# Performance work log

Hardware: AMD Instinct MI355X
Metric: run time of the kernel (lower is better)

## Reference

```python
import jax, jax.numpy as jnp
import numpy as np

D_MODEL = 768
N_HEADS = 12
D_HEAD = D_MODEL // N_HEADS
D_FF = 3072
EPS = 1e-5


def setup_inputs() -> dict:
    key = jax.random.key(0)
    ks = jax.random.split(key, 12)
    s = 0.02
    return {
        "x": jax.random.normal(ks[0], (2, 2048, D_MODEL), dtype=jnp.float32),
        "ln1_g": jnp.ones((D_MODEL,), jnp.float32),
        "ln1_b": jnp.zeros((D_MODEL,), jnp.float32),
        "ln2_g": jnp.ones((D_MODEL,), jnp.float32),
        "ln2_b": jnp.zeros((D_MODEL,), jnp.float32),
        "w_qkv": jax.random.normal(ks[1], (D_MODEL, 3 * D_MODEL), jnp.float32) * s,
        "b_qkv": jnp.zeros((3 * D_MODEL,), jnp.float32),
        "w_out": jax.random.normal(ks[2], (D_MODEL, D_MODEL), jnp.float32) * s,
        "b_out": jnp.zeros((D_MODEL,), jnp.float32),
        "w_fc1": jax.random.normal(ks[3], (D_MODEL, D_FF), jnp.float32) * s,
        "b_fc1": jnp.zeros((D_FF,), jnp.float32),
        "w_fc2": jax.random.normal(ks[4], (D_FF, D_MODEL), jnp.float32) * s,
        "b_fc2": jnp.zeros((D_MODEL,), jnp.float32),
    }


def _layernorm(x, g, b):
    mu = jnp.mean(x, axis=-1, keepdims=True)
    var = jnp.var(x, axis=-1, keepdims=True)
    return (x - mu) * jax.lax.rsqrt(var + EPS) * g + b


def _attention(h, w_qkv, b_qkv, w_out, b_out):
    B, S, _ = h.shape
    qkv = h @ w_qkv + b_qkv  # [B,S,3D]
    qkv = qkv.reshape(B, S, 3, N_HEADS, D_HEAD)
    q, k, v = qkv[:, :, 0], qkv[:, :, 1], qkv[:, :, 2]  # [B,S,H,Dh]
    scale = 1.0 / np.sqrt(D_HEAD).astype(np.float32)
    scores = jnp.einsum("bqhd,bkhd->bhqk", q, k) * scale
    causal = jnp.tril(jnp.ones((S, S), bool))
    scores = jnp.where(causal[None, None], scores, -jnp.inf)
    attn = jax.nn.softmax(scores, axis=-1)
    out = jnp.einsum("bhqk,bkhd->bqhd", attn, v).reshape(B, S, D_MODEL)
    return out @ w_out + b_out


def reference(x, ln1_g, ln1_b, ln2_g, ln2_b, w_qkv, b_qkv, w_out, b_out,
              w_fc1, b_fc1, w_fc2, b_fc2):
    # x = x + Attention(LN1(x))
    x = x + _attention(_layernorm(x, ln1_g, ln1_b), w_qkv, b_qkv, w_out, b_out)
    # x = x + FFN(LN2(x)); GELU is exact (erf) to match torch nn.GELU default
    h = _layernorm(x, ln2_g, ln2_b)
    h = jax.nn.gelu(h @ w_fc1 + b_fc1, approximate=False) @ w_fc2 + b_fc2
    return x + h
```

## Files before the change

### kernel.cpp

```cpp
#include <hip/hip_runtime.h>
#include <hip/hip_bf16.h>

typedef unsigned short u16;
typedef unsigned int u32;
typedef unsigned char u8;
using short8 = __attribute__((ext_vector_type(8))) short;
using f32x4  = __attribute__((ext_vector_type(4))) float;
using float4v = __attribute__((ext_vector_type(4))) float;

__device__ __forceinline__ u16 f2bf(float f) {
    __hip_bfloat16 h = __float2bfloat16(f);
    union { __hip_bfloat16 h; u16 u; } cv; cv.h = h; return cv.u;
}
__device__ __forceinline__ float bf2f(u16 u) {
    union { u32 u; float f; } cv; cv.u = ((u32)u) << 16; return cv.f;
}
__device__ __forceinline__ u16 f2bf_trunc(float f) {
    union { float f; u32 u; } cv; cv.f = f; return (u16)(cv.u >> 16);
}

__device__ __forceinline__ void gload_lds16(const void* g, void* l) {
    __builtin_amdgcn_global_load_lds(
        (const __attribute__((address_space(1))) u32*)g,
        (__attribute__((address_space(3))) u32*)l, 16, 0, 0);
}

__global__ __launch_bounds__(256) void transpose_w(const float* __restrict__ W,
                                                   u16* __restrict__ Wt, int K, int N) {
    __shared__ float tile[32][33];
    int n0 = blockIdx.x * 32, k0 = blockIdx.y * 32;
    int tx = threadIdx.x & 31, ty = threadIdx.x >> 5;
    for (int i = 0; i < 4; i++) {
        int k = ty + i * 8;
        tile[k][tx] = W[(long)(k0 + k) * N + n0 + tx];
    }
    __syncthreads();
    for (int i = 0; i < 4; i++) {
        int n = ty + i * 8;
        Wt[(long)(n0 + n) * K + k0 + tx] = f2bf(tile[tx][n]);
    }
}

__global__ __launch_bounds__(256) void transpose_v(const u16* __restrict__ qkv,
                                                   u16* __restrict__ Vt) {
    __shared__ u16 tile[64][72];
    int s0 = blockIdx.x * 64;
    int bh = blockIdx.y;
    int b = bh / 12, h = bh % 12;
    int tid = threadIdx.x;
    const u16* src = qkv + (long)b * 2048 * 2304 + 1536 + h * 64;
    #pragma unroll
    for (int j = 0; j < 2; ++j) {
        int c = tid + j * 256;
        int srow = c >> 3, ch = c & 7;
        *(short8*)&tile[srow][ch * 8] = *(const short8*)(src + (long)(s0 + srow) * 2304 + ch * 8);
    }
    __syncthreads();
    u16* dst = Vt + (long)bh * 64 * 2048 + s0;
    #pragma unroll
    for (int j = 0; j < 2; ++j) {
        int c = tid + j * 256;
        int d = c >> 3, ch = c & 7;
        short8 v;
        #pragma unroll
        for (int e = 0; e < 8; ++e) v[e] = (short)tile[ch * 8 + e][d];
        *(short8*)(dst + (long)d * 2048 + ch * 8) = v;
    }
}

__global__ __launch_bounds__(256) void ln_kernel(const float* __restrict__ x,
                                                 const float* __restrict__ gain,
                                                 const float* __restrict__ beta,
                                                 u16* __restrict__ out) {
    int row = blockIdx.x;
    const float* xr = x + (long)row * 768;
    int tid = threadIdx.x;
    float v[3];
    float s = 0.f, s2 = 0.f;
    for (int j = 0; j < 3; j++) {
        v[j] = xr[tid + 256 * j];
        s += v[j]; s2 += v[j] * v[j];
    }
    for (int off = 32; off; off >>= 1) {
        s  += __shfl_down(s, off);
        s2 += __shfl_down(s2, off);
    }
    __shared__ float ws[8];
    int lane = tid & 63, w = tid >> 6;
    if (lane == 0) { ws[w] = s; ws[4 + w] = s2; }
    __syncthreads();
    s  = ws[0] + ws[1] + ws[2] + ws[3];
    s2 = ws[4] + ws[5] + ws[6] + ws[7];
    float mu  = s * (1.f / 768.f);
    float var = s2 * (1.f / 768.f) - mu * mu;
    float rs  = rsqrtf(var + 1e-5f);
    for (int j = 0; j < 3; j++) {
        int c = tid + 256 * j;
        out[(long)row * 768 + c] = f2bf((v[j] - mu) * rs * gain[c] + beta[c]);
    }
}

template <int EPI>
__global__ __launch_bounds__(256) void gemm_bf16(const u16* __restrict__ A, int lda,
                                                 const u16* __restrict__ Bt, int ldb,
                                                 const float* __restrict__ bias,
                                                 const float* __restrict__ res,
                                                 void* __restrict__ Cout0,
                                                 void* __restrict__ Cout1,
                                                 int M, int N, int K) {
    __shared__ alignas(16) u16 As[2][128 * 64];
    __shared__ alignas(16) u16 Bs[2][128 * 64];
    int tN = blockIdx.x * 128, tM = blockIdx.y * 128;
    int z = blockIdx.z;
    const u16* Ab = A + (long)z * K;
    const u16* Bb = Bt + (long)z * K;
    void* Cw = z ? Cout1 : Cout0;
    int tid = threadIdx.x;
    int wid = tid >> 6, lane = tid & 63;
    int wm = wid >> 1, wn = wid & 1;
    int g = lane >> 4, r = lane & 15;
    int row0 = tid >> 3, ch = tid & 7;

    f32x4 acc[4][4] = {};
    int KT = K >> 6;

    auto stage = [&](int kt) {
        int k0 = kt << 6;
        u16* ab = As[kt & 1];
        u16* bb = Bs[kt & 1];
        #pragma unroll
        for (int p = 0; p < 4; ++p) {
            int row = p * 32 + row0;
            int slot = ch ^ (row & 7);
            gload_lds16(Ab + (long)(tM + row) * lda + k0 + slot * 8, ab + (p * 256 + wid * 64) * 8);
        }
        #pragma unroll
        for (int p = 0; p < 4; ++p) {
            int row = p * 32 + row0;
            int slot = ch ^ (row & 7);
            gload_lds16(Bb + (long)(tN + row) * ldb + k0 + slot * 8, bb + (p * 256 + wid * 64) * 8);
        }
    };

    stage(0);
    for (int kt = 0; kt < KT; ++kt) {
        if (kt + 1 < KT) {
            stage(kt + 1);
            asm volatile("s_waitcnt vmcnt(8)" ::: "memory");
        } else {
            asm volatile("s_waitcnt vmcnt(0)" ::: "memory");
        }
        __builtin_amdgcn_sched_barrier(0);
        __builtin_amdgcn_s_barrier();
        const u16* ab = As[kt & 1];
        const u16* bb = Bs[kt & 1];

        short8 af[2][4], bf[2][4];
        #pragma unroll
        for (int kh = 0; kh < 2; ++kh)
            #pragma unroll
            for (int mi = 0; mi < 4; ++mi) {
                int row = wm * 64 + mi * 16 + r;
                af[kh][mi] = *(const short8*)(ab + row * 64 + (((kh * 4 + g) ^ (row & 7)) * 8));
            }
        #pragma unroll
        for (int kh = 0; kh < 2; ++kh)
            #pragma unroll
            for (int ni = 0; ni < 4; ++ni) {
                int row = wn * 64 + ni * 16 + r;
                bf[kh][ni] = *(const short8*)(bb + row * 64 + (((kh * 4 + g) ^ (row & 7)) * 8));
            }
        #pragma unroll
        for (int kh = 0; kh < 2; ++kh)
            #pragma unroll
            for (int mi = 0; mi < 4; ++mi)
                #pragma unroll
                for (int ni = 0; ni < 4; ++ni)
                    acc[mi][ni] = __builtin_amdgcn_mfma_f32_16x16x32_bf16(af[kh][mi], bf[kh][ni], acc[mi][ni], 0, 0, 0);
        __builtin_amdgcn_s_barrier();
    }

    #pragma unroll
    for (int mi = 0; mi < 4; mi++) {
        #pragma unroll
        for (int ni = 0; ni < 4; ni++) {
            int col = tN + wn * 64 + ni * 16 + r;
            float bv = (EPI == 3) ? 0.f : bias[col];
            #pragma unroll
            for (int reg = 0; reg < 4; reg++) {
                int row = tM + wm * 64 + mi * 16 + g * 4 + reg;
                float v = acc[mi][ni][reg] + bv;
                if (EPI == 1) {
                    v += res[(long)row * N + col];
                    ((float*)Cw)[(long)row * N + col] = v;
                } else if (EPI == 2) {
                    v = 0.5f * v * (1.f + erff(v * 0.70710678118f));
                    ((u16*)Cw)[(long)row * N + col] = f2bf(v);
                } else if (EPI == 3) {
                    ((float*)Cw)[(long)row * N + col] = v;
                } else {
                    ((u16*)Cw)[(long)row * N + col] = f2bf(v);
                }
            }
        }
    }
}

__global__ __launch_bounds__(192) void fc2_combine(const float* __restrict__ P0,
                                                   const float* __restrict__ P1,
                                                   const float* __restrict__ bias,
                                                   const float* __restrict__ res,
                                                   float* __restrict__ out) {
    long row = blockIdx.x;
    int c = threadIdx.x * 4;
    long i = row * 768 + c;
    float4v a = *(const float4v*)(P0 + i);
    float4v b = *(const float4v*)(P1 + i);
    float4v bs = *(const float4v*)(bias + c);
    float4v rr = *(const float4v*)(res + i);
    float4v o = a + b + bs + rr;
    *(float4v*)(out + i) = o;
}

__device__ __constant__ u8 SLOT_QI[40] = {
    15,15,15,15, 14,14,14, 13,13,13, 12,12,12, 11,11,11, 10,10, 9,9, 8,8, 7,7, 6, 5, 4, 3,
    14,10,6,2,  13,9,5,1,  12,8,4,0 };
__device__ __constant__ u8 SLOT_C[40] = {
    0,1,2,3, 0,1,2, 0,1,2, 0,1,2, 0,1,2, 0,1, 0,1, 0,1, 0,1, 0, 0, 0, 0,
    3,2,1,0, 3,2,1,0, 3,2,1,0 };

__global__ __launch_bounds__(256) void attn_kernel(const u16* __restrict__ qkv,
                                                   const u16* __restrict__ Vt,
                                                   u16* __restrict__ Opart,
                                                   float* __restrict__ Ml) {
    __shared__ alignas(16) u16 Ks[2 * 64 * 64];
    __shared__ alignas(16) u16 Vs[2 * 64 * 64];
    __shared__ alignas(16) u16 Ps[4 * 32 * 64];
    int flat = blockIdx.x;
    int s = flat / 24, bh = flat % 24;
    int qi = SLOT_QI[s], c = SLOT_C[s];
    int b = bh / 12, h = bh % 12;
    int tid = threadIdx.x;
    int w = tid >> 6, lane = tid & 63;
    int g = lane >> 4, r = lane & 15;
    int qt0 = qi * 128;
    int qw0 = qt0 + w * 32;
    int kvbase = c * 512;
    int nit = (c < (qi >> 2)) ? 8 : (2 * (qi & 3) + 2);
    const u16* base = qkv + (long)b * 2048 * 2304;
    const u16* Qb = base + h * 64;
    const u16* Kb = base + 768 + h * 64;
    const u16* Vtb = Vt + (long)bh * 64 * 2048;

    const float SC = 0.125f * 1.44269504f;
    short8 qf[2][2];
    #pragma unroll
    for (int fi = 0; fi < 2; ++fi) {
        const u16* qrow = Qb + (long)(qw0 + fi * 16 + r) * 2304;
        qf[fi][0] = *(const short8*)(qrow + 8 * g);
        qf[fi][1] = *(const short8*)(qrow + 32 + 8 * g);
        #pragma unroll
        for (int kh = 0; kh < 2; ++kh)
            #pragma unroll
            for (int j = 0; j < 8; ++j)
                qf[fi][kh][j] = (short)f2bf(bf2f((u16)qf[fi][kh][j]) * SC);
    }

    f32x4 oacc[2][4] = {};
    float mrow[2][4], psum[2][4];
    #pragma unroll
    for (int fi = 0; fi < 2; ++fi)
        #pragma unroll
        for (int i = 0; i < 4; i++) { mrow[fi][i] = 8.0f; psum[fi][i] = 0.f; }

    auto stage = [&](int kt) {
        int kv0 = kvbase + kt * 64;
        u16* kb = Ks + (kt & 1) * 4096;
        u16* vb = Vs + (kt & 1) * 4096;
        #pragma unroll
        for (int j = 0; j < 2; ++j) {
            int cc = w * 128 + j * 64 + lane;
            int row = cc >> 3;
            int slot = (cc & 7) ^ (row & 7);
            gload_lds16(Kb + (long)(kv0 + row) * 2304 + slot * 8, kb + (w * 128 + j * 64) * 8);
            gload_lds16(Vtb + (long)row * 2048 + kv0 + slot * 8, vb + (w * 128 + j * 64) * 8);
        }
    };

    stage(0);
    for (int kt = 0; kt < nit; ++kt) {
        int kv0 = kvbase + kt * 64;
        if (kt + 1 < nit) {
            stage(kt + 1);
            asm volatile("s_waitcnt vmcnt(4)" ::: "memory");
        } else {
            asm volatile("s_waitcnt vmcnt(0)" ::: "memory");
        }
        __builtin_amdgcn_sched_barrier(0);
        __builtin_amdgcn_s_barrier();
        const u16* kb = Ks + (kt & 1) * 4096;
        const u16* vb = Vs + (kt & 1) * 4096;

        bool act0 = kv0 <= qw0 + 15;
        bool act1 = kv0 <= qw0 + 31;

        f32x4 sc[2][4] = {};
        if (act1) {
            #pragma unroll
            for (int nt = 0; nt < 4; ++nt)
                #pragma unroll
                for (int kh = 0; kh < 2; ++kh) {
                    short8 bk = *(const short8*)(kb + (nt * 16 + r) * 64 + ((kh * 32 + g * 8) ^ ((r & 7) << 3)));
                    sc[1][nt] = __builtin_amdgcn_mfma_f32_16x16x32_bf16(qf[1][kh], bk, sc[1][nt], 0, 0, 0);
                    if (act0)
                        sc[0][nt] = __builtin_amdgcn_mfma_f32_16x16x32_bf16(qf[0][kh], bk, sc[0][nt], 0, 0, 0);
                }

            #pragma unroll
            for (int fi = 0; fi < 2; ++fi) {
                if (fi == 0 && !act0) continue;
                if ((kv0 + 63) > (qw0 + fi * 16)) {
                    #pragma unroll
                    for (int nt = 0; nt < 4; ++nt)
                        #pragma unroll
                        for (int reg = 0; reg < 4; ++reg)
                            if ((kv0 + nt * 16 + r) > (qw0 + fi * 16 + g * 4 + reg))
                                sc[fi][nt][reg] = -1e30f;
                }
            }

            float tl[2][4];
            bool need = false;
            #pragma unroll
            for (int fi = 0; fi < 2; ++fi) {
                if (fi == 0 && !act0) continue;
                #pragma unroll
                for (int reg = 0; reg < 4; ++reg) {
                    tl[fi][reg] = fmaxf(fmaxf(sc[fi][0][reg], sc[fi][1][reg]),
                                        fmaxf(sc[fi][2][reg], sc[fi][3][reg]));
                    need = need || (tl[fi][reg] > mrow[fi][reg] + 8.f);
                }
            }
            if (__any(need)) {
                #pragma unroll
                for (int fi = 0; fi < 2; ++fi) {
                    if (fi == 0 && !act0) continue;
                    #pragma unroll
                    for (int reg = 0; reg < 4; ++reg) {
                        float rm = tl[fi][reg];
                        #pragma unroll
                        for (int off = 1; off < 16; off <<= 1)
                            rm = fmaxf(rm, __shfl_xor(rm, off));
                        float mnew = fmaxf(mrow[fi][reg], rm);
                        float alpha = exp2f(mrow[fi][reg] - mnew);
                        mrow[fi][reg] = mnew;
                        psum[fi][reg] *= alpha;
                        #pragma unroll
                        for (int dt = 0; dt < 4; ++dt) oacc[fi][dt][reg] *= alpha;
                    }
                }
            }

            #pragma unroll
            for (int fi = 0; fi < 2; ++fi) {
                if (fi == 0 && !act0) continue;
                u16* Pw = Ps + (w * 32 + fi * 16) * 64;
                #pragma unroll
                for (int nt = 0; nt < 4; ++nt)
                    #pragma unroll
                    for (int reg = 0; reg < 4; ++reg) {
                        float p = exp2f(sc[fi][nt][reg] - mrow[fi][reg]);
                        psum[fi][reg] += p;
                        int row = g * 4 + reg;
                        Pw[row * 64 + ((nt * 16 + r) ^ ((row & 7) << 3))] = f2bf_trunc(p);
                    }
            }

            short8 pf[2][2];
            #pragma unroll
            for (int fi = 0; fi < 2; ++fi) {
                if (fi == 0 && !act0) continue;
                const u16* Pw = Ps + (w * 32 + fi * 16) * 64;
                pf[fi][0] = *(const short8*)(Pw + r * 64 + ((g * 8) ^ ((r & 7) << 3)));
                pf[fi][1] = *(const short8*)(Pw + r * 64 + ((32 + g * 8) ^ ((r & 7) << 3)));
            }
            #pragma unroll
            for (int dt = 0; dt < 4; ++dt)
                #pragma unroll
                for (int kc = 0; kc < 2; ++kc) {
                    short8 vf = *(const short8*)(vb + (dt * 16 + r) * 64 + ((kc * 32 + g * 8) ^ ((r & 7) << 3)));
                    oacc[1][dt] = __builtin_amdgcn_mfma_f32_16x16x32_bf16(pf[1][kc], vf, oacc[1][dt], 0, 0, 0);
                    if (act0)
                        oacc[0][dt] = __builtin_amdgcn_mfma_f32_16x16x32_bf16(pf[0][kc], vf, oacc[0][dt], 0, 0, 0);
                }
        }
        __builtin_amdgcn_s_barrier();
    }

    float lrow[2][4];
    #pragma unroll
    for (int fi = 0; fi < 2; ++fi)
        #pragma unroll
        for (int reg = 0; reg < 4; ++reg) {
            float l = psum[fi][reg];
            #pragma unroll
            for (int off = 1; off < 16; off <<= 1)
                l += __shfl_xor(l, off);
            lrow[fi][reg] = l;
        }

    long pbase = ((long)c * 24 + bh) * 2048;
    #pragma unroll
    for (int fi = 0; fi < 2; ++fi)
        #pragma unroll
        for (int dt = 0; dt < 4; ++dt)
            #pragma unroll
            for (int reg = 0; reg < 4; ++reg) {
                int q = qw0 + fi * 16 + g * 4 + reg;
                int d = dt * 16 + r;
                Opart[(pbase + q) * 64 + d] = f2bf(oacc[fi][dt][reg]);
            }
    if (r == 0) {
        #pragma unroll
        for (int fi = 0; fi < 2; ++fi)
            #pragma unroll
            for (int reg = 0; reg < 4; ++reg) {
                int q = qw0 + fi * 16 + g * 4 + reg;
                Ml[(pbase + q) * 2]     = mrow[fi][reg];
                Ml[(pbase + q) * 2 + 1] = lrow[fi][reg];
            }
    }
}

__global__ __launch_bounds__(256) void attn_combine(const u16* __restrict__ Opart,
                                                    const float* __restrict__ Ml,
                                                    u16* __restrict__ Ob) {
    int bh = blockIdx.y;
    int b = bh / 12, h = bh % 12;
    int q = blockIdx.x * 4 + (threadIdx.x >> 6);
    int d = threadIdx.x & 63;
    int qi = q >> 7;
    int nact = (qi >> 2) + 1;
    float mv[4], lv[4];
    float M = -1e30f;
    for (int c = 0; c < nact; ++c) {
        long base = ((long)c * 24 + bh) * 2048 + q;
        mv[c] = Ml[base * 2];
        lv[c] = Ml[base * 2 + 1];
        M = fmaxf(M, mv[c]);
    }
    float denom = 0.f, val = 0.f;
    for (int c = 0; c < nact; ++c) {
        float wgt = exp2f(mv[c] - M);
        denom += lv[c] * wgt;
        val += wgt * bf2f(Opart[(((long)c * 24 + bh) * 2048 + q) * 64 + d]);
    }
    Ob[((long)b * 2048 + q) * 768 + h * 64 + d] = f2bf(val / denom);
}

extern "C" void kernel_launch(void* const* d_in, const int* in_sizes, int n_in,
                              void* d_out, int out_size, void* d_ws, size_t ws_size,
                              hipStream_t stream) {
    const float* x     = (const float*)d_in[0];
    const float* ln1_g = (const float*)d_in[1];
    const float* ln1_b = (const float*)d_in[2];
    const float* ln2_g = (const float*)d_in[3];
    const float* ln2_b = (const float*)d_in[4];
    const float* w_qkv = (const float*)d_in[5];
    const float* b_qkv = (const float*)d_in[6];
    const float* w_out = (const float*)d_in[7];
    const float* b_out = (const float*)d_in[8];
    const float* w_fc1 = (const float*)d_in[9];
    const float* b_fc1 = (const float*)d_in[10];
    const float* w_fc2 = (const float*)d_in[11];
    const float* b_fc2 = (const float*)d_in[12];

    char* ws = (char*)d_ws;
    size_t off = 0;
    auto alloc = [&](size_t bytes) { void* p = ws + off; off += (bytes + 255) & ~255ULL; return p; };
    u16* h1    = (u16*)alloc(4096UL * 768 * 2);
    u16* WqkvT = (u16*)alloc(2304UL * 768 * 2);
    u16* WoutT = (u16*)alloc(768UL * 768 * 2);
    u16* Wfc1T = (u16*)alloc(3072UL * 768 * 2);
    u16* Wfc2T = (u16*)alloc(768UL * 3072 * 2);
    u16* qkvb  = (u16*)alloc(4096UL * 2304 * 2);
    u16* Vtb   = (u16*)alloc(24UL * 64 * 2048 * 2);
    u16* Ob    = (u16*)alloc(4096UL * 768 * 2);
    float* x2  = (float*)alloc(4096UL * 768 * 4);
    char* pool = (char*)alloc(4096UL * 768 * 2 + 4096UL * 3072 * 2);
    u16* h2      = (u16*)pool;
    u16* gbuf    = (u16*)(pool + 4096UL * 768 * 2);
    u16* Opart   = (u16*)pool;
    float* Ml    = (float*)(pool + 4UL * 24 * 2048 * 64 * 2);
    float* P0 = (float*)qkvb;
    float* P1 = (float*)h1;

    transpose_w<<<dim3(2304 / 32, 768 / 32), 256, 0, stream>>>(w_qkv, WqkvT, 768, 2304);
    transpose_w<<<dim3(768 / 32, 768 / 32), 256, 0, stream>>>(w_out, WoutT, 768, 768);
    transpose_w<<<dim3(3072 / 32, 768 / 32), 256, 0, stream>>>(w_fc1, Wfc1T, 768, 3072);
    transpose_w<<<dim3(768 / 32, 3072 / 32), 256, 0, stream>>>(w_fc2, Wfc2T, 3072, 768);

    ln_kernel<<<4096, 256, 0, stream>>>(x, ln1_g, ln1_b, h1);
    gemm_bf16<0><<<dim3(18, 32, 1), 256, 0, stream>>>(h1, 768, WqkvT, 768, b_qkv, nullptr, qkvb, nullptr, 4096, 2304, 768);
    transpose_v<<<dim3(32, 24), 256, 0, stream>>>(qkvb, Vtb);
    attn_kernel<<<dim3(960), 256, 0, stream>>>(qkvb, Vtb, Opart, Ml);
    attn_combine<<<dim3(512, 24), 256, 0, stream>>>(Opart, Ml, Ob);
    gemm_bf16<1><<<dim3(6, 32, 1), 256, 0, stream>>>(Ob, 768, WoutT, 768, b_out, x, x2, nullptr, 4096, 768, 768);
    ln_kernel<<<4096, 256, 0, stream>>>(x2, ln2_g, ln2_b, h2);
    gemm_bf16<2><<<dim3(24, 32, 1), 256, 0, stream>>>(h2, 768, Wfc1T, 768, b_fc1, nullptr, gbuf, nullptr, 4096, 3072, 768);
    gemm_bf16<3><<<dim3(6, 32, 2), 256, 0, stream>>>(gbuf, 3072, Wfc2T, 3072, nullptr, nullptr, P0, P1, 4096, 768, 1536);
    fc2_combine<<<4096, 192, 0, stream>>>(P0, P1, b_fc2, x2, (float*)d_out);
}
```

Before: 225.6 us.

## Split attention KV into finer 256-key chunks and transpose score MFMA layout

Attention work is split into 256-key chunks instead of 512, raising the grid from 960 to 1728 blocks. Partial outputs are stored per slot, and the combine kernel looks each one up through a new slot table. The score MFMA operands are swapped so each lane holds one query row. This makes row max and row sum cheaper to compute and lets P be written to LDS as packed 64-bit stores. s_setprio is also added around the MFMA sections. The aim is better load balance and fewer shuffles, at the cost of more partials for the combine step to read and merge.

```diff
diff --git a/kernel.cpp b/kernel.cpp
--- a/kernel.cpp
+++ b/kernel.cpp
@@ -7,6 +7,7 @@
 using short8 = __attribute__((ext_vector_type(8))) short;
 using f32x4  = __attribute__((ext_vector_type(4))) float;
 using float4v = __attribute__((ext_vector_type(4))) float;
+using u32x2  = __attribute__((ext_vector_type(2))) unsigned int;
 
 __device__ __forceinline__ u16 f2bf(float f) {
     __hip_bfloat16 h = __float2bfloat16(f);
@@ -15,8 +16,8 @@
 __device__ __forceinline__ float bf2f(u16 u) {
     union { u32 u; float f; } cv; cv.u = ((u32)u) << 16; return cv.f;
 }
-__device__ __forceinline__ u16 f2bf_trunc(float f) {
-    union { float f; u32 u; } cv; cv.f = f; return (u16)(cv.u >> 16);
+__device__ __forceinline__ u32 fbits(float f) {
+    union { float f; u32 u; } cv; cv.f = f; return cv.u;
 }
 
 __device__ __forceinline__ void gload_lds16(const void* g, void* l) {
@@ -222,12 +223,57 @@
     *(float4v*)(out + i) = o;
 }
 
-__device__ __constant__ u8 SLOT_QI[40] = {
-    15,15,15,15, 14,14,14, 13,13,13, 12,12,12, 11,11,11, 10,10, 9,9, 8,8, 7,7, 6, 5, 4, 3,
-    14,10,6,2,  13,9,5,1,  12,8,4,0 };
-__device__ __constant__ u8 SLOT_C[40] = {
-    0,1,2,3, 0,1,2, 0,1,2, 0,1,2, 0,1,2, 0,1, 0,1, 0,1, 0,1, 0, 0, 0, 0,
-    3,2,1,0, 3,2,1,0, 3,2,1,0 };
+__device__ __constant__ u8 SLOT_QI[72] = {
+ 15,15,15,15,15,15,15,15,
+ 14,14,14,14,14,14,14,
+ 13,13,13,13,13,13,13,
+ 12,12,12,12,12,12,
+ 11,11,11,11,11,11,
+ 10,10,10,10,10,
+ 9,9,9,9,9,
+ 8,8,8,8,
+ 7,7,7,7,
+ 6,6,6,
+ 5,5,5,
+ 4,4,
+ 3,3,
+ 2,
+ 1,
+ 14,12,10,8,6,4,2,0 };
+__device__ __constant__ u8 SLOT_C[72] = {
+ 0,1,2,3,4,5,6,7,
+ 0,1,2,3,4,5,6,
+ 0,1,2,3,4,5,6,
+ 0,1,2,3,4,5,
+ 0,1,2,3,4,5,
+ 0,1,2,3,4,
+ 0,1,2,3,4,
+ 0,1,2,3,
+ 0,1,2,3,
+ 0,1,2,
+ 0,1,2,
+ 0,1,
+ 0,1,
+ 0,
+ 0,
+ 7,6,5,4,3,2,1,0 };
+__device__ __constant__ u8 SLOT_OF[16][8] = {
+ {71,0,0,0,0,0,0,0},
+ {63,0,0,0,0,0,0,0},
+ {62,70,0,0,0,0,0,0},
+ {60,61,0,0,0,0,0,0},
+ {58,59,69,0,0,0,0,0},
+ {55,56,57,0,0,0,0,0},
+ {52,53,54,68,0,0,0,0},
+ {48,49,50,51,0,0,0,0},
+ {44,45,46,47,67,0,0,0},
+ {39,40,41,42,43,0,0,0},
+ {34,35,36,37,38,66,0,0},
+ {28,29,30,31,32,33,0,0},
+ {22,23,24,25,26,27,65,0},
+ {15,16,17,18,19,20,21,0},
+ {8,9,10,11,12,13,14,64},
+ {0,1,2,3,4,5,6,7} };
 
 __global__ __launch_bounds__(256) void attn_kernel(const u16* __restrict__ qkv,
                                                    const u16* __restrict__ Vt,
@@ -245,8 +291,8 @@
     int g = lane >> 4, r = lane & 15;
     int qt0 = qi * 128;
     int qw0 = qt0 + w * 32;
-    int kvbase = c * 512;
-    int nit = (c < (qi >> 2)) ? 8 : (2 * (qi & 3) + 2);
+    int kvbase = c * 256;
+    int nit = 2 * (qi + 1) - 4 * c; if (nit > 4) nit = 4;
     const u16* base = qkv + (long)b * 2048 * 2304;
     const u16* Qb = base + h * 64;
     const u16* Kb = base + 768 + h * 64;
@@ -267,11 +313,8 @@
     }
 
     f32x4 oacc[2][4] = {};
-    float mrow[2][4], psum[2][4];
-    #pragma unroll
-    for (int fi = 0; fi < 2; ++fi)
-        #pragma unroll
-        for (int i = 0; i < 4; i++) { mrow[fi][i] = 8.0f; psum[fi][i] = 0.f; }
+    float mrow[2] = {8.0f, 8.0f};
+    float ps0[2] = {0.f, 0.f}, ps1[2] = {0.f, 0.f};
 
     auto stage = [&](int kt) {
         int kv0 = kvbase + kt * 64;
@@ -304,59 +347,62 @@
         bool act0 = kv0 <= qw0 + 15;
         bool act1 = kv0 <= qw0 + 31;
 
-        f32x4 sc[2][4] = {};
         if (act1) {
+            f32x4 sc[2][4] = {};
+            __builtin_amdgcn_s_setprio(1);
             #pragma unroll
             for (int nt = 0; nt < 4; ++nt)
                 #pragma unroll
                 for (int kh = 0; kh < 2; ++kh) {
                     short8 bk = *(const short8*)(kb + (nt * 16 + r) * 64 + ((kh * 32 + g * 8) ^ ((r & 7) << 3)));
-                    sc[1][nt] = __builtin_amdgcn_mfma_f32_16x16x32_bf16(qf[1][kh], bk, sc[1][nt], 0, 0, 0);
+                    sc[1][nt] = __builtin_amdgcn_mfma_f32_16x16x32_bf16(bk, qf[1][kh], sc[1][nt], 0, 0, 0);
                     if (act0)
-                        sc[0][nt] = __builtin_amdgcn_mfma_f32_16x16x32_bf16(qf[0][kh], bk, sc[0][nt], 0, 0, 0);
+                        sc[0][nt] = __builtin_amdgcn_mfma_f32_16x16x32_bf16(bk, qf[0][kh], sc[0][nt], 0, 0, 0);
                 }
+            __builtin_amdgcn_s_setprio(0);
 
             #pragma unroll
             for (int fi = 0; fi < 2; ++fi) {
                 if (fi == 0 && !act0) continue;
                 if ((kv0 + 63) > (qw0 + fi * 16)) {
+                    int q = qw0 + fi * 16 + r;
                     #pragma unroll
                     for (int nt = 0; nt < 4; ++nt)
                         #pragma unroll
                         for (int reg = 0; reg < 4; ++reg)
-                            if ((kv0 + nt * 16 + r) > (qw0 + fi * 16 + g * 4 + reg))
+                            if ((kv0 + nt * 16 + g * 4 + reg) > q)
                                 sc[fi][nt][reg] = -1e30f;
                 }
             }
 
-            float tl[2][4];
+            float tl[2];
             bool need = false;
             #pragma unroll
             for (int fi = 0; fi < 2; ++fi) {
                 if (fi == 0 && !act0) continue;
-                #pragma unroll
-                for (int reg = 0; reg < 4; ++reg) {
-                    tl[fi][reg] = fmaxf(fmaxf(sc[fi][0][reg], sc[fi][1][reg]),
-                                        fmaxf(sc[fi][2][reg], sc[fi][3][reg]));
-                    need = need || (tl[fi][reg] > mrow[fi][reg] + 8.f);
-                }
+                float m0 = fmaxf(fmaxf(sc[fi][0][0], sc[fi][0][1]), fmaxf(sc[fi][0][2], sc[fi][0][3]));
+                float m1 = fmaxf(fmaxf(sc[fi][1][0], sc[fi][1][1]), fmaxf(sc[fi][1][2], sc[fi][1][3]));
+                float m2 = fmaxf(fmaxf(sc[fi][2][0], sc[fi][2][1]), fmaxf(sc[fi][2][2], sc[fi][2][3]));
+                float m3 = fmaxf(fmaxf(sc[fi][3][0], sc[fi][3][1]), fmaxf(sc[fi][3][2], sc[fi][3][3]));
+                tl[fi] = fmaxf(fmaxf(m0, m1), fmaxf(m2, m3));
+                need = need || (tl[fi] > mrow[fi] + 8.f);
             }
             if (__any(need)) {
                 #pragma unroll
                 for (int fi = 0; fi < 2; ++fi) {
                     if (fi == 0 && !act0) continue;
+                    float rm = tl[fi];
+                    rm = fmaxf(rm, __shfl_xor(rm, 16));
+                    rm = fmaxf(rm, __shfl_xor(rm, 32));
+                    float mnew = fmaxf(mrow[fi], rm);
+                    float alpha = exp2f(mrow[fi] - mnew);
+                    mrow[fi] = mnew;
+                    ps0[fi] *= alpha; ps1[fi] *= alpha;
                     #pragma unroll
                     for (int reg = 0; reg < 4; ++reg) {
-                        float rm = tl[fi][reg];
+                        float ar = __shfl(alpha, (lane & 48) | (g * 4 + reg));
                         #pragma unroll
-                        for (int off = 1; off < 16; off <<= 1)
-                            rm = fmaxf(rm, __shfl_xor(rm, off));
-                        float mnew = fmaxf(mrow[fi][reg], rm);
-                        float alpha = exp2f(mrow[fi][reg] - mnew);
-                        mrow[fi][reg] = mnew;
-                        psum[fi][reg] *= alpha;
-                        #pragma unroll
-                        for (int dt = 0; dt < 4; ++dt) oacc[fi][dt][reg] *= alpha;
+                        for (int dt = 0; dt < 4; ++dt) oacc[fi][dt][reg] *= ar;
                     }
                 }
             }
@@ -364,26 +410,31 @@
             #pragma unroll
             for (int fi = 0; fi < 2; ++fi) {
                 if (fi == 0 && !act0) continue;
-                u16* Pw = Ps + (w * 32 + fi * 16) * 64;
+                u16* Pr = Ps + (w * 32 + fi * 16 + r) * 64;
                 #pragma unroll
-                for (int nt = 0; nt < 4; ++nt)
-                    #pragma unroll
-                    for (int reg = 0; reg < 4; ++reg) {
-                        float p = exp2f(sc[fi][nt][reg] - mrow[fi][reg]);
-                        psum[fi][reg] += p;
-                        int row = g * 4 + reg;
-                        Pw[row * 64 + ((nt * 16 + r) ^ ((row & 7) << 3))] = f2bf_trunc(p);
-                    }
+                for (int nt = 0; nt < 4; ++nt) {
+                    float p0 = exp2f(sc[fi][nt][0] - mrow[fi]);
+                    float p1 = exp2f(sc[fi][nt][1] - mrow[fi]);
+                    float p2 = exp2f(sc[fi][nt][2] - mrow[fi]);
+                    float p3 = exp2f(sc[fi][nt][3] - mrow[fi]);
+                    ps0[fi] += p0 + p2;
+                    ps1[fi] += p1 + p3;
+                    u32 lo = __builtin_amdgcn_perm(fbits(p1), fbits(p0), 0x07060302);
+                    u32 hi = __builtin_amdgcn_perm(fbits(p3), fbits(p2), 0x07060302);
+                    int col = (nt * 16 + g * 4) ^ ((r & 7) << 3);
+                    *(u32x2*)(Pr + col) = u32x2{lo, hi};
+                }
             }
 
             short8 pf[2][2];
             #pragma unroll
             for (int fi = 0; fi < 2; ++fi) {
                 if (fi == 0 && !act0) continue;
-                const u16* Pw = Ps + (w * 32 + fi * 16) * 64;
-                pf[fi][0] = *(const short8*)(Pw + r * 64 + ((g * 8) ^ ((r & 7) << 3)));
-                pf[fi][1] = *(const short8*)(Pw + r * 64 + ((32 + g * 8) ^ ((r & 7) << 3)));
-            }
+                const u16* Pr = Ps + (w * 32 + fi * 16 + r) * 64;
+                pf[fi][0] = *(const short8*)(Pr + ((g * 8) ^ ((r & 7) << 3)));
+                pf[fi][1] = *(const short8*)(Pr + ((32 + g * 8) ^ ((r & 7) << 3)));
+            }
+            __builtin_amdgcn_s_setprio(1);
             #pragma unroll
             for (int dt = 0; dt < 4; ++dt)
                 #pragma unroll
@@ -393,42 +444,38 @@
                     if (act0)
                         oacc[0][dt] = __builtin_amdgcn_mfma_f32_16x16x32_bf16(pf[0][kc], vf, oacc[0][dt], 0, 0, 0);
                 }
+            __builtin_amdgcn_s_setprio(0);
         }
         __builtin_amdgcn_s_barrier();
     }
 
-    float lrow[2][4];
+    float lrow[2];
+    #pragma unroll
+    for (int fi = 0; fi < 2; ++fi) {
+        float l = ps0[fi] + ps1[fi];
+        l += __shfl_xor(l, 16);
+        l += __shfl_xor(l, 32);
+        lrow[fi] = l;
+    }
+
+    long pbase = ((long)s * 24 + bh) * 128;
     #pragma unroll
     for (int fi = 0; fi < 2; ++fi)
         #pragma unroll
-        for (int reg = 0; reg < 4; ++reg) {
-            float l = psum[fi][reg];
-            #pragma unroll
-            for (int off = 1; off < 16; off <<= 1)
-                l += __shfl_xor(l, off);
-            lrow[fi][reg] = l;
-        }
-
-    long pbase = ((long)c * 24 + bh) * 2048;
-    #pragma unroll
-    for (int fi = 0; fi < 2; ++fi)
-        #pragma unroll
         for (int dt = 0; dt < 4; ++dt)
             #pragma unroll
             for (int reg = 0; reg < 4; ++reg) {
-                int q = qw0 + fi * 16 + g * 4 + reg;
+                int lq = w * 32 + fi * 16 + g * 4 + reg;
                 int d = dt * 16 + r;
-                Opart[(pbase + q) * 64 + d] = f2bf(oacc[fi][dt][reg]);
-            }
-    if (r == 0) {
-        #pragma unroll
-        for (int fi = 0; fi < 2; ++fi)
-            #pragma unroll
-            for (int reg = 0; reg < 4; ++reg) {
-                int q = qw0 + fi * 16 + g * 4 + reg;
-                Ml[(pbase + q) * 2]     = mrow[fi][reg];
-                Ml[(pbase + q) * 2 + 1] = lrow[fi][reg];
-            }
+                Opart[(pbase + lq) * 64 + d] = f2bf(oacc[fi][dt][reg]);
+            }
+    if ((lane & 48) == 0) {
+        #pragma unroll
+        for (int fi = 0; fi < 2; ++fi) {
+            int lq = w * 32 + fi * 16 + r;
+            Ml[(pbase + lq) * 2]     = mrow[fi];
+            Ml[(pbase + lq) * 2 + 1] = lrow[fi];
+        }
     }
 }
 
@@ -440,11 +487,15 @@
     int q = blockIdx.x * 4 + (threadIdx.x >> 6);
     int d = threadIdx.x & 63;
     int qi = q >> 7;
-    int nact = (qi >> 2) + 1;
-    float mv[4], lv[4];
+    int lq = q & 127;
+    int nact = (qi >> 1) + 1;
+    float mv[8], lv[8];
+    u8 sl[8];
     float M = -1e30f;
     for (int c = 0; c < nact; ++c) {
-        long base = ((long)c * 24 + bh) * 2048 + q;
+        u8 s = SLOT_OF[qi][c];
+        sl[c] = s;
+        long base = ((long)s * 24 + bh) * 128 + lq;
         mv[c] = Ml[base * 2];
         lv[c] = Ml[base * 2 + 1];
         M = fmaxf(M, mv[c]);
@@ -453,7 +504,7 @@
     for (int c = 0; c < nact; ++c) {
         float wgt = exp2f(mv[c] - M);
         denom += lv[c] * wgt;
-        val += wgt * bf2f(Opart[(((long)c * 24 + bh) * 2048 + q) * 64 + d]);
+        val += wgt * bf2f(Opart[((((long)sl[c] * 24 + bh) * 128) + lq) * 64 + d]);
     }
     Ob[((long)b * 2048 + q) * 768 + h * 64 + d] = f2bf(val / denom);
 }
@@ -491,7 +542,7 @@
     u16* h2      = (u16*)pool;
     u16* gbuf    = (u16*)(pool + 4096UL * 768 * 2);
     u16* Opart   = (u16*)pool;
-    float* Ml    = (float*)(pool + 4UL * 24 * 2048 * 64 * 2);
+    float* Ml    = (float*)(pool + 72UL * 24 * 128 * 64 * 2);
     float* P0 = (float*)qkvb;
     float* P1 = (float*)h1;
 
@@ -503,7 +554,7 @@
     ln_kernel<<<4096, 256, 0, stream>>>(x, ln1_g, ln1_b, h1);
     gemm_bf16<0><<<dim3(18, 32, 1), 256, 0, stream>>>(h1, 768, WqkvT, 768, b_qkv, nullptr, qkvb, nullptr, 4096, 2304, 768);
     transpose_v<<<dim3(32, 24), 256, 0, stream>>>(qkvb, Vtb);
-    attn_kernel<<<dim3(960), 256, 0, stream>>>(qkvb, Vtb, Opart, Ml);
+    attn_kernel<<<dim3(1728), 256, 0, stream>>>(qkvb, Vtb, Opart, Ml);
     attn_combine<<<dim3(512, 24), 256, 0, stream>>>(Opart, Ml, Ob);
     gemm_bf16<1><<<dim3(6, 32, 1), 256, 0, stream>>>(Ob, 768, WoutT, 768, b_out, x, x2, nullptr, 4096, 768, 768);
     ln_kernel<<<4096, 256, 0, stream>>>(x2, ln2_g, ln2_b, h2);
```

Result: slower. 244.6 us (+8.4%).
